# Optimization experiments

Hardware: AMD Instinct MI355X
Metric: run time of the kernel (lower is better)

Reference implementation:

```python
import jax, jax.numpy as jnp
import numpy as np

N_NODES = 100000
N_EDGES = 1000000
D_IN = 64
FEATURES = [64, 64, 16]


def setup_inputs() -> dict:
    key = jax.random.key(0)
    ks = jax.random.split(key, 10)
    nodes = jax.random.normal(ks[0], (N_NODES, D_IN), dtype=jnp.float32)
    senders = jax.random.randint(ks[1], (N_EDGES,), 0, N_NODES, dtype=jnp.int64)
    receivers = jax.random.randint(ks[2], (N_EDGES,), 0, N_NODES, dtype=jnp.int64)
    dims = [D_IN] + FEATURES
    params = {}
    for i in range(len(FEATURES)):
        fan_in = dims[i]
        # hk.Linear default: truncated-normal-ish init; plain normal scaled is fine for a reference
        params[f"W{i}"] = jax.random.normal(ks[3 + i], (dims[i], dims[i + 1]), dtype=jnp.float32) / np.sqrt(fan_in)
        params[f"b{i}"] = jnp.zeros((dims[i + 1],), dtype=jnp.float32)
    return {"nodes": nodes, "senders": senders, "receivers": receivers, **params}


def _gcn_layer(h, senders, receivers, W, b, use_tanh, add_self_edges):
    N = h.shape[0]
    h = h @ W + b
    if use_tanh:
        h = jnp.tanh(h)
    if add_self_edges:
        self_idx = jnp.arange(N, dtype=senders.dtype)
        s = jnp.concatenate([senders, self_idx], axis=0)
        r = jnp.concatenate([receivers, self_idx], axis=0)
    else:
        s, r = senders, receivers
    ones = jnp.ones(s.shape, dtype=h.dtype)
    deg_s = jax.ops.segment_sum(ones, s, num_segments=N)
    deg_r = jax.ops.segment_sum(ones, r, num_segments=N)
    h = h * jax.lax.rsqrt(jnp.maximum(deg_s, 1.0))[:, None]
    h = jax.ops.segment_sum(h[s], r, num_segments=N)  # gather -> scatter-add
    h = h * jax.lax.rsqrt(jnp.maximum(deg_r, 1.0))[:, None]
    return h


def reference(nodes, senders, receivers, W0, b0, W1, b1, W2, b2):
    h = nodes
    # layers over features[:-1]: tanh activation, self edges added
    h = _gcn_layer(h, senders, receivers, W0, b0, use_tanh=True, add_self_edges=True)
    h = _gcn_layer(h, senders, receivers, W1, b1, use_tanh=True, add_self_edges=True)
    # final layer: linear only, no self edges, still symmetric normalization
    h = _gcn_layer(h, senders, receivers, W2, b2, use_tanh=False, add_self_edges=False)
    return h
```

## Files before the change

kernel.cpp:

```cpp
#include <hip/hip_runtime.h>


#define CAP 32
#define BSH 7
#define BW 128
#define BCAP 1664
#define EPT 4

typedef unsigned short u16;
typedef unsigned int u32;

__device__ __forceinline__ float bf2f(u16 u) {
    return __uint_as_float(((u32)u) << 16);
}
__device__ __forceinline__ u16 f2bf(float f) {
    u32 x = __float_as_uint(f);
    u32 r = x + 0x7fff + ((x >> 16) & 1);
    return (u16)(r >> 16);
}
__device__ __forceinline__ float fast_tanh(float x) {
    x = fminf(15.f, fmaxf(-15.f, x));
    float e = __expf(2.f * x);
    return (e - 1.f) / (e + 1.f);
}
__device__ __forceinline__ int unpack_deg(const u32* pk, int n) {
    return (int)((pk[n >> 2] >> (8 * (n & 3))) & 255u);
}

__global__ __launch_bounds__(256) void k_init(int* __restrict__ curR,
                                              int* __restrict__ curS, int nbuk) {
    int t = blockIdx.x * 256 + threadIdx.x;
    if (t < nbuk) {
        curR[t] = t * BCAP;
        curS[t] = t * BCAP;
    }
}

__global__ __launch_bounds__(1024) void k_part(const int* __restrict__ s,
                                               const int* __restrict__ r,
                                               int* __restrict__ curR,
                                               int* __restrict__ curS,
                                               int2* __restrict__ pairR,
                                               int* __restrict__ svalS,
                                               int E, int nbuk) {
    __shared__ int cR[1024], cS[1024], bR[1024], bS[1024];
    const int t = threadIdx.x;
    for (int i = t; i < nbuk; i += 1024) { cR[i] = 0; cS[i] = 0; }
    __syncthreads();

    int ss[EPT], rr[EPT];
    const int base = blockIdx.x * (1024 * EPT);
#pragma unroll
    for (int i = 0; i < EPT; ++i) {
        int e = base + i * 1024 + t;
        ss[i] = (e < E) ? s[e] : -1;
        rr[i] = (e < E) ? r[e] : -1;
    }
#pragma unroll
    for (int i = 0; i < EPT; ++i) {
        if (rr[i] >= 0) {
            atomicAdd(&cR[rr[i] >> BSH], 1);
            atomicAdd(&cS[ss[i] >> BSH], 1);
        }
    }
    __syncthreads();
    for (int i = t; i < nbuk; i += 1024) {
        bR[i] = cR[i] ? atomicAdd(&curR[i], cR[i]) : 0;
        bS[i] = cS[i] ? atomicAdd(&curS[i], cS[i]) : 0;
    }
    __syncthreads();
    for (int i = t; i < nbuk; i += 1024) { cR[i] = 0; cS[i] = 0; }
    __syncthreads();
#pragma unroll
    for (int i = 0; i < EPT; ++i) {
        if (rr[i] >= 0) {
            int rb = rr[i] >> BSH;
            int pos = bR[rb] + atomicAdd(&cR[rb], 1);
            if (pos < (rb + 1) * BCAP) pairR[pos] = make_int2(ss[i], rr[i]);
            int sb = ss[i] >> BSH;
            int ps = bS[sb] + atomicAdd(&cS[sb], 1);
            if (ps < (sb + 1) * BCAP) svalS[ps] = ss[i];
        }
    }
}

__global__ __launch_bounds__(256) void k_ellb(const int2* __restrict__ pairR,
                                              const int* __restrict__ curR,
                                              int* __restrict__ ell,
                                              u32* __restrict__ degIp) {
    __shared__ int degLoc[BW];
    const int b = blockIdx.x, t = threadIdx.x;
    if (t < BW) degLoc[t] = 0;
    __syncthreads();
    const int start = b * BCAP;
    const int cnt = min(curR[b] - start, BCAP);
    for (int e = t; e < cnt; e += 256) {
        int2 p = pairR[start + e];
        int slot = atomicAdd(&degLoc[p.y - (b << BSH)], 1);
        if (slot < CAP) ell[p.y * CAP + slot] = p.x;
    }
    __syncthreads();
    if (t < BW / 4) {
        u32 w = (u32)min(degLoc[4 * t], 255) |
                ((u32)min(degLoc[4 * t + 1], 255) << 8) |
                ((u32)min(degLoc[4 * t + 2], 255) << 16) |
                ((u32)min(degLoc[4 * t + 3], 255) << 24);
        degIp[(b << (BSH - 2)) + t] = w;
    }
}

__global__ __launch_bounds__(256) void k_dego(const int* __restrict__ svalS,
                                              const int* __restrict__ curS,
                                              u32* __restrict__ degOp) {
    __shared__ int degLoc[BW];
    const int b = blockIdx.x, t = threadIdx.x;
    if (t < BW) degLoc[t] = 0;
    __syncthreads();
    const int start = b * BCAP;
    const int cnt = min(curS[b] - start, BCAP);
    for (int e = t; e < cnt; e += 256) {
        atomicAdd(&degLoc[svalS[start + e] - (b << BSH)], 1);
    }
    __syncthreads();
    if (t < BW / 4) {
        u32 w = (u32)min(degLoc[4 * t], 255) |
                ((u32)min(degLoc[4 * t + 1], 255) << 8) |
                ((u32)min(degLoc[4 * t + 2], 255) << 16) |
                ((u32)min(degLoc[4 * t + 3], 255) << 24);
        degOp[(b << (BSH - 2)) + t] = w;
    }
}

__global__ __launch_bounds__(256, 4) void k_transform64(const float* __restrict__ in,
                                                        const float* __restrict__ W,
                                                        const float* __restrict__ b,
                                                        const u32* __restrict__ degOp,
                                                        u16* __restrict__ out, int N) {
    __shared__ float4 lds[4][128];
    const int lane = threadIdx.x & 63;
    const int wv = threadIdx.x >> 6;

    float wc[64];
#pragma unroll
    for (int k = 0; k < 64; ++k) wc[k] = W[k * 64 + lane];
    const float bias = b[lane];

    const int base = blockIdx.x * 32 + wv * 8;
    const float4* in4 = (const float4*)in;
#pragma unroll
    for (int r2 = 0; r2 < 2; ++r2) {
        int idx = r2 * 64 + lane;
        int nn = base + (idx >> 4);
        float4 v = {0.f, 0.f, 0.f, 0.f};
        if (nn < N) v = in4[(size_t)base * 16 + idx];
        lds[wv][idx] = v;
    }
#pragma unroll
    for (int i = 0; i < 8; ++i) {
        const int n = base + i;
        if (n >= N) break;
        float acc = 0.f;
#pragma unroll
        for (int kk = 0; kk < 16; ++kk) {
            float4 h = lds[wv][i * 16 + kk];
            acc = fmaf(h.x, wc[4 * kk + 0], acc);
            acc = fmaf(h.y, wc[4 * kk + 1], acc);
            acc = fmaf(h.z, wc[4 * kk + 2], acc);
            acc = fmaf(h.w, wc[4 * kk + 3], acc);
        }
        float as01 = rsqrtf((float)unpack_deg(degOp, n) + 1.f);
        acc = fast_tanh(acc + bias) * as01;
        out[(size_t)n * 64 + lane] = f2bf(acc);
    }
}

__global__ __launch_bounds__(256, 4) void k_fgt64(const u16* __restrict__ h,
                                                  const u32* __restrict__ degOp,
                                                  const u32* __restrict__ degIp,
                                                  const int* __restrict__ ell,
                                                  const float* __restrict__ W,
                                                  const float* __restrict__ b,
                                                  u16* __restrict__ y, int N) {
    __shared__ float4 lds[4][16];
    const int lane = threadIdx.x & 63;
    const int wv = threadIdx.x >> 6;
    const int g = lane >> 4, c = lane & 15;

    float wc[64];
#pragma unroll
    for (int k = 0; k < 64; ++k) wc[k] = W[k * 64 + lane];
    const float bias = b[lane];

    const ushort4* h4 = (const ushort4*)h;
    const int base = blockIdx.x * 32 + wv * 8;
    for (int i8 = 0; i8 < 8; ++i8) {
        const int n = base + i8;
        if (n >= N) break;
        const int di = unpack_deg(degIp, n);
        const int deg = min(di, CAP);
        int idxv = (lane < CAP) ? ell[n * CAP + lane] : 0;

        float4 acc = {0.f, 0.f, 0.f, 0.f};
        const int jn = (deg + 3) >> 2;
        for (int j = 0; j < jn; ++j) {
            int i = g + 4 * j;
            int id = __shfl(idxv, i, 64);
            if (i < deg) {
                ushort4 v = h4[(size_t)id * 16 + c];
                acc.x += bf2f(v.x); acc.y += bf2f(v.y);
                acc.z += bf2f(v.z); acc.w += bf2f(v.w);
            }
        }
#pragma unroll
        for (int m = 16; m <= 32; m <<= 1) {
            acc.x += __shfl_xor(acc.x, m, 64);
            acc.y += __shfl_xor(acc.y, m, 64);
            acc.z += __shfl_xor(acc.z, m, 64);
            acc.w += __shfl_xor(acc.w, m, 64);
        }
        ushort4 sv = h4[(size_t)n * 16 + c];
        acc.x += bf2f(sv.x); acc.y += bf2f(sv.y);
        acc.z += bf2f(sv.z); acc.w += bf2f(sv.w);
        if (g == 0) lds[wv][c] = acc;

        const float inscale = rsqrtf((float)di + 1.f);
        const float outscale = rsqrtf((float)unpack_deg(degOp, n) + 1.f);
        float dot = 0.f;
        const float* row = (const float*)lds[wv];
#pragma unroll
        for (int k = 0; k < 64; k += 4) {
            float4 hh = *(const float4*)(row + k);
            dot = fmaf(hh.x, wc[k + 0], dot);
            dot = fmaf(hh.y, wc[k + 1], dot);
            dot = fmaf(hh.z, wc[k + 2], dot);
            dot = fmaf(hh.w, wc[k + 3], dot);
        }
        float v = fast_tanh(fmaf(dot, inscale, bias)) * outscale;
        y[(size_t)n * 64 + lane] = f2bf(v);
    }
}

__global__ __launch_bounds__(256, 4) void k_fgt16(const u16* __restrict__ h,
                                                  const u32* __restrict__ degOp,
                                                  const u32* __restrict__ degIp,
                                                  const int* __restrict__ ell,
                                                  const float* __restrict__ W,
                                                  const float* __restrict__ b,
                                                  u16* __restrict__ y16, int N) {
    __shared__ float4 lds[4][16];
    const int lane = threadIdx.x & 63;
    const int wv = threadIdx.x >> 6;
    const int g = lane >> 4, c = lane & 15;
    const int j = lane & 15;

    float wc[16];
#pragma unroll
    for (int kk = 0; kk < 16; ++kk) wc[kk] = W[(16 * g + kk) * 16 + j];
    const float bias = b[j];

    const ushort4* h4 = (const ushort4*)h;
    const int base = blockIdx.x * 32 + wv * 8;
    for (int i8 = 0; i8 < 8; ++i8) {
        const int n = base + i8;
        if (n >= N) break;
        const int di = unpack_deg(degIp, n);
        const int deg = min(di, CAP);
        int idxv = (lane < CAP) ? ell[n * CAP + lane] : 0;

        float4 acc = {0.f, 0.f, 0.f, 0.f};
        const int jn = (deg + 3) >> 2;
        for (int jj = 0; jj < jn; ++jj) {
            int i = g + 4 * jj;
            int id = __shfl(idxv, i, 64);
            if (i < deg) {
                ushort4 v = h4[(size_t)id * 16 + c];
                acc.x += bf2f(v.x); acc.y += bf2f(v.y);
                acc.z += bf2f(v.z); acc.w += bf2f(v.w);
            }
        }
#pragma unroll
        for (int m = 16; m <= 32; m <<= 1) {
            acc.x += __shfl_xor(acc.x, m, 64);
            acc.y += __shfl_xor(acc.y, m, 64);
            acc.z += __shfl_xor(acc.z, m, 64);
            acc.w += __shfl_xor(acc.w, m, 64);
        }
        ushort4 sv = h4[(size_t)n * 16 + c];
        acc.x += bf2f(sv.x); acc.y += bf2f(sv.y);
        acc.z += bf2f(sv.z); acc.w += bf2f(sv.w);
        if (g == 0) lds[wv][c] = acc;

        const float* row = (const float*)lds[wv];
        float dot = 0.f;
#pragma unroll
        for (int kk = 0; kk < 16; ++kk) dot = fmaf(row[16 * g + kk], wc[kk], dot);
#pragma unroll
        for (int m = 16; m <= 32; m <<= 1) dot += __shfl_xor(dot, m, 64);

        if (g == 0) {
            const float inscale = rsqrtf((float)di + 1.f);
            const float outscale = rsqrtf(fmaxf((float)unpack_deg(degOp, n), 1.f));
            float v = fmaf(dot, inscale, bias) * outscale;
            y16[(size_t)n * 16 + j] = f2bf(v);
        }
    }
}

__global__ __launch_bounds__(256) void k_g16(const u16* __restrict__ h,
                                             const u32* __restrict__ degIp,
                                             const int* __restrict__ ell,
                                             float* __restrict__ out, int N) {
    const int lane = threadIdx.x & 63;
    const int wv = threadIdx.x >> 6;
    const int n = blockIdx.x * 4 + wv;
    if (n >= N) return;
    const int g = lane >> 2, c = lane & 3;
    const int di = unpack_deg(degIp, n);
    const int deg = min(di, CAP);
    int idxv = (lane < CAP) ? ell[n * CAP + lane] : 0;

    const ushort4* h4 = (const ushort4*)h;
    float4 acc = {0.f, 0.f, 0.f, 0.f};
    const int jn = (deg + 15) >> 4;
    for (int j = 0; j < jn; ++j) {
        int i = g + 16 * j;
        int id = __shfl(idxv, i, 64);
        if (i < deg) {
            ushort4 v = h4[(size_t)id * 4 + c];
            acc.x += bf2f(v.x); acc.y += bf2f(v.y);
            acc.z += bf2f(v.z); acc.w += bf2f(v.w);
        }
    }
#pragma unroll
    for (int m = 4; m <= 32; m <<= 1) {
        acc.x += __shfl_xor(acc.x, m, 64);
        acc.y += __shfl_xor(acc.y, m, 64);
        acc.z += __shfl_xor(acc.z, m, 64);
        acc.w += __shfl_xor(acc.w, m, 64);
    }
    if (g == 0) {
        float sc = rsqrtf(fmaxf((float)di, 1.f));
        acc.x *= sc; acc.y *= sc; acc.z *= sc; acc.w *= sc;
        ((float4*)out)[(size_t)n * 4 + c] = acc;
    }
}

extern "C" void kernel_launch(void* const* d_in, const int* in_sizes, int n_in,
                              void* d_out, int out_size, void* d_ws, size_t ws_size,
                              hipStream_t stream) {
    const float* nodes = (const float*)d_in[0];
    const int* senders = (const int*)d_in[1];
    const int* receivers = (const int*)d_in[2];
    const float* W0 = (const float*)d_in[3];
    const float* b0 = (const float*)d_in[4];
    const float* W1 = (const float*)d_in[5];
    const float* b1 = (const float*)d_in[6];
    const float* W2 = (const float*)d_in[7];
    const float* b2 = (const float*)d_in[8];
    float* out = (float*)d_out;

    const int N = in_sizes[0] / 64;
    const int E = in_sizes[1];
    const int nbuk = (N + BW - 1) >> BSH;
    const int nwords = nbuk * (BW / 4);

    u16* A = (u16*)d_ws;
    u16* B = A + (size_t)N * 64;
    u16* Y16 = B + (size_t)N * 64;
    u32* degOp = (u32*)(Y16 + (size_t)N * 16);
    u32* degIp = degOp + nwords;
    int* curR = (int*)(degIp + nwords);
    int* curS = curR + nbuk;
    int* ell = (int*)(curS + nbuk);
    int2* pairR = (int2*)(ell + (size_t)N * CAP);
    int* svalS = (int*)(pairR + (size_t)nbuk * BCAP);

    k_init<<<(nbuk + 255) / 256, 256, 0, stream>>>(curR, curS, nbuk);
    const int pblk = (E + 1024 * EPT - 1) / (1024 * EPT);
    k_part<<<pblk, 1024, 0, stream>>>(senders, receivers, curR, curS,
                                      pairR, svalS, E, nbuk);
    k_ellb<<<nbuk, 256, 0, stream>>>(pairR, curR, ell, degIp);
    k_dego<<<nbuk, 256, 0, stream>>>(svalS, curS, degOp);

    const int tb = (N + 31) / 32;
    const int fb = (N + 31) / 32;
    const int gb = (N + 3) / 4;

    k_transform64<<<tb, 256, 0, stream>>>(nodes, W0, b0, degOp, A, N);
    k_fgt64<<<fb, 256, 0, stream>>>(A, degOp, degIp, ell, W1, b1, B, N);
    k_fgt16<<<fb, 256, 0, stream>>>(B, degOp, degIp, ell, W2, b2, Y16, N);
    k_g16<<<gb, 256, 0, stream>>>(Y16, degIp, ell, out, N);
}
```

Measured before the change: 276.4 us.

## Gather one feature per lane and broadcast via readlane instead of LDS

Restructures the 64-wide fused gather-transform kernel so each lane accumulates one feature column over all neighbors, reading neighbor indices as wave-uniform scalar loads with 4-way unrolling. The LDS staging and cross-group shuffle reduction are replaced by 64 readlane broadcasts feeding the matvec. This removes shuffles, LDS traffic and the partial-lane gather split. The trade-off is narrower 2-byte per-lane loads instead of 8-byte vector loads, more serial iterations per neighbor, and 64 readlane instructions per node.

New measurement: 278.5 us. No clear change (+0.8%).

```diff
diff --git a/kernel.cpp b/kernel.cpp
--- a/kernel.cpp
+++ b/kernel.cpp
@@ -181,59 +181,53 @@
                                                   const float* __restrict__ W,
                                                   const float* __restrict__ b,
                                                   u16* __restrict__ y, int N) {
-    __shared__ float4 lds[4][16];
     const int lane = threadIdx.x & 63;
-    const int wv = threadIdx.x >> 6;
-    const int g = lane >> 4, c = lane & 15;
+    const int wv = __builtin_amdgcn_readfirstlane(threadIdx.x >> 6);
 
     float wc[64];
 #pragma unroll
     for (int k = 0; k < 64; ++k) wc[k] = W[k * 64 + lane];
     const float bias = b[lane];
 
-    const ushort4* h4 = (const ushort4*)h;
     const int base = blockIdx.x * 32 + wv * 8;
     for (int i8 = 0; i8 < 8; ++i8) {
         const int n = base + i8;
         if (n >= N) break;
         const int di = unpack_deg(degIp, n);
         const int deg = min(di, CAP);
-        int idxv = (lane < CAP) ? ell[n * CAP + lane] : 0;
-
-        float4 acc = {0.f, 0.f, 0.f, 0.f};
-        const int jn = (deg + 3) >> 2;
-        for (int j = 0; j < jn; ++j) {
-            int i = g + 4 * j;
-            int id = __shfl(idxv, i, 64);
-            if (i < deg) {
-                ushort4 v = h4[(size_t)id * 16 + c];
-                acc.x += bf2f(v.x); acc.y += bf2f(v.y);
-                acc.z += bf2f(v.z); acc.w += bf2f(v.w);
-            }
-        }
-#pragma unroll
-        for (int m = 16; m <= 32; m <<= 1) {
-            acc.x += __shfl_xor(acc.x, m, 64);
-            acc.y += __shfl_xor(acc.y, m, 64);
-            acc.z += __shfl_xor(acc.z, m, 64);
-            acc.w += __shfl_xor(acc.w, m, 64);
-        }
-        ushort4 sv = h4[(size_t)n * 16 + c];
-        acc.x += bf2f(sv.x); acc.y += bf2f(sv.y);
-        acc.z += bf2f(sv.z); acc.w += bf2f(sv.w);
-        if (g == 0) lds[wv][c] = acc;
+        const int* __restrict__ rowp = ell + (size_t)n * CAP;
+
+        float acc = 0.f;
+        int e = 0;
+        for (; e + 4 <= deg; e += 4) {
+            int i0 = rowp[e + 0];
+            int i1 = rowp[e + 1];
+            int i2 = rowp[e + 2];
+            int i3 = rowp[e + 3];
+            u16 a0 = h[(size_t)i0 * 64 + lane];
+            u16 a1 = h[(size_t)i1 * 64 + lane];
+            u16 a2 = h[(size_t)i2 * 64 + lane];
+            u16 a3 = h[(size_t)i3 * 64 + lane];
+            acc += bf2f(a0);
+            acc += bf2f(a1);
+            acc += bf2f(a2);
+            acc += bf2f(a3);
+        }
+        for (; e < deg; ++e) {
+            int id = rowp[e];
+            acc += bf2f(h[(size_t)id * 64 + lane]);
+        }
+        acc += bf2f(h[(size_t)n * 64 + lane]);
 
         const float inscale = rsqrtf((float)di + 1.f);
         const float outscale = rsqrtf((float)unpack_deg(degOp, n) + 1.f);
+
         float dot = 0.f;
-        const float* row = (const float*)lds[wv];
-#pragma unroll
-        for (int k = 0; k < 64; k += 4) {
-            float4 hh = *(const float4*)(row + k);
-            dot = fmaf(hh.x, wc[k + 0], dot);
-            dot = fmaf(hh.y, wc[k + 1], dot);
-            dot = fmaf(hh.z, wc[k + 2], dot);
-            dot = fmaf(hh.w, wc[k + 3], dot);
+#pragma unroll
+        for (int k = 0; k < 64; ++k) {
+            float rv = __uint_as_float(
+                __builtin_amdgcn_readlane(__float_as_uint(acc), k));
+            dot = fmaf(rv, wc[k], dot);
         }
         float v = fast_tanh(fmaf(dot, inscale, bias)) * outscale;
         y[(size_t)n * 64 + lane] = f2bf(v);
```
